# Kernel optimization log

Measured on AMD Instinct MI355X. Metric: run time of the kernel, lower is better.

## Reference

```python
import jax, jax.numpy as jnp
import numpy as np

N_ENT = 50000     # n_entities
C = 128           # channel
N_EDGES = 1600000 # n_edges (avg degree 32)
N_REL = 11        # n_relations; edge_type in [1, N_REL-1]
N_HOPS = 3
EPS = 1e-12       # F.normalize default eps


def setup_inputs() -> dict:
    key = jax.random.key(0)
    k1, k2, k3, k4 = jax.random.split(key, 4)
    entity_emb = jax.random.normal(k1, (N_ENT, C), dtype=jnp.float32)
    edge_index = jax.random.randint(k2, (2, N_EDGES), 0, N_ENT, dtype=jnp.int64)
    edge_type = jax.random.randint(k3, (N_EDGES,), 1, N_REL, dtype=jnp.int64)
    # xavier_uniform bound for (N_REL-1, C)
    bound = float(np.sqrt(6.0 / ((N_REL - 1) + C)))
    weight = jax.random.uniform(k4, (N_REL - 1, C), jnp.float32, -bound, bound)
    return {"entity_emb": entity_emb, "edge_index": edge_index,
            "edge_type": edge_type, "weight": weight}


def reference(entity_emb, edge_index, edge_type, weight):
    head, tail = edge_index[0], edge_index[1]
    # relation embedding per edge: weight[edge_type - 1] -> [E, C]
    rel_emb = weight[edge_type - 1]
    ones = jnp.ones((edge_index.shape[1],), entity_emb.dtype)
    # per-head in-degree counts (constant across hops)
    cnt = jax.ops.segment_sum(ones, head, num_segments=N_ENT)
    denom = jnp.maximum(cnt, 1.0)[:, None]  # scatter_mean: zero rows stay zero

    def hop(emb):
        msg = emb[tail] * rel_emb                                   # gather + mul [E, C]
        agg = jax.ops.segment_sum(msg, head, num_segments=N_ENT) / denom  # scatter_mean
        # F.normalize (L2 per row)
        norm = jnp.linalg.norm(agg, axis=1, keepdims=True)
        return agg / jnp.maximum(norm, EPS)

    res = entity_emb
    emb = entity_emb
    for _ in range(N_HOPS):
        emb = hop(emb)
        res = res + emb
    return res
```

## Files before the change

kernel.cpp:

```cpp
#include <hip/hip_runtime.h>

#define N_ENT   50000
#define CH      128
#define N_EDGES 1600000
#define N_RELM1 10
#define NB      391
#define BCAP    4608
#define BCAP_P  8192
#define PART_BLOCKS 800
#define CHUNK   (N_EDGES / PART_BLOCKS)
#define NRG     (N_ENT / 4)
#define NKEY    512
#define EPS_N   1e-12f

#define RFL(x) __builtin_amdgcn_readfirstlane(x)

__device__ __forceinline__ unsigned int f2bf_bits(float f) {
    unsigned int x = __float_as_uint(f);
    return (x + 0x7FFFu + ((x >> 16) & 1u)) >> 16;
}

__global__ __launch_bounds__(256) void gc_part_kernel(const int* __restrict__ head,
                                                      const int* __restrict__ tail,
                                                      const int* __restrict__ etyp,
                                                      int* __restrict__ barr,
                                                      int* __restrict__ pack,
                                                      const float* __restrict__ ent,
                                                      unsigned int* __restrict__ emb) {
    __shared__ int hist[512];
    __shared__ int boff_s[512];
    __shared__ int fctr[512];
    __shared__ int psum[256];
    __shared__ int stageE[CHUNK];
    __shared__ unsigned short stageB[CHUNK];
    __shared__ int stage2[CHUNK];
    int tid = threadIdx.x, blk = blockIdx.x;
    for (int i = tid; i < 512; i += 256) { hist[i] = 0; fctr[i] = 0; }
    __syncthreads();
    int lo = blk * CHUNK;
    for (int i = tid; i < CHUNK; i += 256) {
        int e = lo + i;
        int h = head[e];
        int b = h >> 7;
        stageE[i] = (tail[e] & 0xFFFF) | ((etyp[e] - 1) << 16) | ((h & 127) << 20);
        stageB[i] = (unsigned short)b;
        atomicAdd(&hist[b], 1);
    }
    __syncthreads();
    int a0 = hist[2 * tid], a1 = hist[2 * tid + 1];
    int s2 = a0 + a1;
    psum[tid] = s2;
    __syncthreads();
    for (int d = 1; d < 256; d <<= 1) {
        int t = (tid >= d) ? psum[tid - d] : 0;
        __syncthreads();
        psum[tid] += t;
        __syncthreads();
    }
    int excl = psum[tid] - s2;
    boff_s[2 * tid] = excl;
    boff_s[2 * tid + 1] = excl + a0;
    __syncthreads();
    for (int i = tid; i < CHUNK; i += 256) {
        int b = stageB[i];
        int pos = boff_s[b] + atomicAdd(&fctr[b], 1);
        stage2[pos] = stageE[i];
    }
    __syncthreads();
    for (int i = tid; i < CHUNK; i += 256) barr[lo + i] = stage2[i];
    for (int i = tid; i < NB; i += 256)
        pack[blk * NB + i] = (boff_s[i] << 8) | fctr[i];
    for (int i = blk * 256 + tid; i < N_ENT * (CH / 2); i += PART_BLOCKS * 256) {
        float2 v = *(const float2*)(ent + 2 * (size_t)i);
        emb[i] = f2bf_bits(v.x) | (f2bf_bits(v.y) << 16);
    }
}

__global__ __launch_bounds__(1024) void gc_place_kernel(const int* __restrict__ barr,
                                                        const int* __restrict__ pack,
                                                        int* __restrict__ deg_arr,
                                                        int* __restrict__ rg_off,
                                                        int* __restrict__ cpk,
                                                        int* __restrict__ csr) {
    __shared__ int ent_s[BCAP];
    __shared__ int psum[1024];
    __shared__ int kcnt[NKEY];
    __shared__ int kctr[NKEY];
    __shared__ int kbase[NKEY];
    int b = blockIdx.x, tid = threadIdx.x;
    if (tid < NKEY) { kcnt[tid] = 0; kctr[tid] = 0; }
    int c = 0, o = 0;
    if (tid < PART_BLOCKS) {
        int pk = pack[tid * NB + b];
        c = pk & 255;
        o = pk >> 8;
    }
    psum[tid] = c;
    __syncthreads();
    for (int d = 1; d < 1024; d <<= 1) {
        int t = (tid >= d) ? psum[tid - d] : 0;
        __syncthreads();
        psum[tid] += t;
        __syncthreads();
    }
    int my_off = psum[tid] - c;
    int n = psum[1023];
    const int* src = barr + tid * CHUNK + o;
    for (int k = 0; k < c; ++k) ent_s[my_off + k] = src[k];
    __syncthreads();
    for (int i = tid; i < n; i += 1024) {
        int e = ent_s[i];
        int hl = (e >> 20) & 127;
        int key = ((hl >> 2) << 4) | (((e >> 14) & 3) << 2) | (hl & 3);
        atomicAdd(&kcnt[key], 1);
    }
    __syncthreads();
    if (tid < 128) {
        int rgl = tid >> 2, r = tid & 3;
        int base = (rgl << 4) | r;
        int c0 = kcnt[base], c1 = kcnt[base + 4], c2 = kcnt[base + 8], c3 = kcnt[base + 12];
        int h = (b << 7) + tid;
        if (h < N_ENT) {
            deg_arr[h] = c0 + c1 + c2 + c3;
            cpk[(((b << 5) + rgl) << 2) + r] =
                ((c0 + 7) >> 3) | (((c1 + 7) >> 3) << 8) |
                (((c2 + 7) >> 3) << 16) | (((c3 + 7) >> 3) << 24);
        }
    }
    int a0 = 0, a1 = 0, s2 = 0;
    if (tid < 256) {
        a0 = (kcnt[2 * tid] + 7) & ~7;
        a1 = (kcnt[2 * tid + 1] + 7) & ~7;
        s2 = a0 + a1;
        psum[tid] = s2;
    }
    __syncthreads();
    for (int d = 1; d < 256; d <<= 1) {
        int t = (tid < 256 && tid >= d) ? psum[tid - d] : 0;
        __syncthreads();
        if (tid < 256) psum[tid] += t;
        __syncthreads();
    }
    if (tid < 256) {
        int excl = psum[tid] - s2;
        kbase[2 * tid] = excl;
        kbase[2 * tid + 1] = excl + a0;
    }
    __syncthreads();
    int lo = b * BCAP_P;
    if (tid < 32) {
        int grg = (b << 5) + tid;
        if (grg < NRG) rg_off[grg] = lo + kbase[tid << 4];
    }
    for (int i = tid; i < n; i += 1024) {
        int e = ent_s[i];
        int hl = (e >> 20) & 127;
        int key = ((hl >> 2) << 4) | (((e >> 14) & 3) << 2) | (hl & 3);
        int pos = lo + kbase[key] + atomicAdd(&kctr[key], 1);
        csr[pos] = e & 0xFFFFF;
    }
    __syncthreads();
    if (tid < NKEY) {
        int cc = kcnt[tid];
        int pc = (cc + 7) & ~7;
        int p0 = lo + kbase[tid];
        for (int k = cc; k < pc; ++k) csr[p0 + k] = 15 << 16;
    }
}

__global__ __launch_bounds__(256, 8) void gc_hop_kernel(
        const unsigned int* __restrict__ src,
        const int* __restrict__ deg_arr,
        const int* __restrict__ rg_off,
        const int* __restrict__ cpk,
        const int* __restrict__ csr,
        const float* __restrict__ wt,
        unsigned int* __restrict__ dst,
        float* __restrict__ res,
        const float* __restrict__ ent,
        const unsigned int* __restrict__ yprev,
        int mode) {
    __shared__ float wt_s[16 * CH];
    for (int i = threadIdx.x; i < 16 * CH; i += 256)
        wt_s[i] = (i < N_RELM1 * CH) ? wt[i] : 0.f;
    __syncthreads();

    int wave = threadIdx.x >> 6, lane = threadIdx.x & 63;
    int rg = RFL(blockIdx.x * 4 + wave);
    if (rg >= NRG) return;

    int4 dd = ((const int4*)deg_arr)[rg];
    int4 cc = ((const int4*)cpk)[rg];
    int segv = rg_off[rg];

    int D0 = RFL(dd.x), D1 = RFL(dd.y), D2 = RFL(dd.z), D3 = RFL(dd.w);
    int C0 = RFL(cc.x), C1 = RFL(cc.y), C2 = RFL(cc.z), C3 = RFL(cc.w);
    int seg = RFL(segv);

    const int4* mp = (const int4*)(csr + seg);
    int4 mB0 = mp[0], mB1 = mp[1];
    mp += 2;

    float ax0 = 0.f, ay0 = 0.f, ax1 = 0.f, ay1 = 0.f;
    float ax2 = 0.f, ay2 = 0.f, ax3 = 0.f, ay3 = 0.f;

    const unsigned* srcl = src + lane;
    const float2*   wl   = (const float2*)wt_s + lane;

#define CHUNK8(axr, ayr) { \
    int p0_ = RFL(mB0.x), p1_ = RFL(mB0.y), p2_ = RFL(mB0.z), p3_ = RFL(mB0.w); \
    int p4_ = RFL(mB1.x), p5_ = RFL(mB1.y), p6_ = RFL(mB1.z), p7_ = RFL(mB1.w); \
    mB0 = mp[0]; mB1 = mp[1]; mp += 2; \
    unsigned v0_ = srcl[(unsigned)(p0_ & 0xFFFF) * 64u]; \
    unsigned v1_ = srcl[(unsigned)(p1_ & 0xFFFF) * 64u]; \
    unsigned v2_ = srcl[(unsigned)(p2_ & 0xFFFF) * 64u]; \
    unsigned v3_ = srcl[(unsigned)(p3_ & 0xFFFF) * 64u]; \
    unsigned v4_ = srcl[(unsigned)(p4_ & 0xFFFF) * 64u]; \
    unsigned v5_ = srcl[(unsigned)(p5_ & 0xFFFF) * 64u]; \
    unsigned v6_ = srcl[(unsigned)(p6_ & 0xFFFF) * 64u]; \
    unsigned v7_ = srcl[(unsigned)(p7_ & 0xFFFF) * 64u]; \
    float2 w0_ = wl[((p0_ >> 16) & 15) * 64]; \
    float2 w1_ = wl[((p1_ >> 16) & 15) * 64]; \
    float2 w2_ = wl[((p2_ >> 16) & 15) * 64]; \
    float2 w3_ = wl[((p3_ >> 16) & 15) * 64]; \
    float2 w4_ = wl[((p4_ >> 16) & 15) * 64]; \
    float2 w5_ = wl[((p5_ >> 16) & 15) * 64]; \
    float2 w6_ = wl[((p6_ >> 16) & 15) * 64]; \
    float2 w7_ = wl[((p7_ >> 16) & 15) * 64]; \
    axr = fmaf(__uint_as_float(v0_ << 16), w0_.x, axr); \
    ayr = fmaf(__uint_as_float(v0_ & 0xFFFF0000u), w0_.y, ayr); \
    axr = fmaf(__uint_as_float(v1_ << 16), w1_.x, axr); \
    ayr = fmaf(__uint_as_float(v1_ & 0xFFFF0000u), w1_.y, ayr); \
    axr = fmaf(__uint_as_float(v2_ << 16), w2_.x, axr); \
    ayr = fmaf(__uint_as_float(v2_ & 0xFFFF0000u), w2_.y, ayr); \
    axr = fmaf(__uint_as_float(v3_ << 16), w3_.x, axr); \
    ayr = fmaf(__uint_as_float(v3_ & 0xFFFF0000u), w3_.y, ayr); \
    axr = fmaf(__uint_as_float(v4_ << 16), w4_.x, axr); \
    ayr = fmaf(__uint_as_float(v4_ & 0xFFFF0000u), w4_.y, ayr); \
    axr = fmaf(__uint_as_float(v5_ << 16), w5_.x, axr); \
    ayr = fmaf(__uint_as_float(v5_ & 0xFFFF0000u), w5_.y, ayr); \
    axr = fmaf(__uint_as_float(v6_ << 16), w6_.x, axr); \
    ayr = fmaf(__uint_as_float(v6_ & 0xFFFF0000u), w6_.y, ayr); \
    axr = fmaf(__uint_as_float(v7_ << 16), w7_.x, axr); \
    ayr = fmaf(__uint_as_float(v7_ & 0xFFFF0000u), w7_.y, ayr); \
}

#define RUN(axr, ayr, Cr) { \
    int n_ = (Cr >> sh) & 255; \
    for (int c_ = 0; c_ < n_; ++c_) CHUNK8(axr, ayr) \
}

    for (int g2 = 0; g2 < 4; ++g2) {
        int sh = g2 << 3;
        RUN(ax0, ay0, C0)
        RUN(ax1, ay1, C1)
        RUN(ax2, ay2, C2)
        RUN(ax3, ay3, C3)
    }
#undef RUN
#undef CHUNK8

#define ROWOUT(r, axr, ayr, Dr) { \
        int row = (rg << 2) + r; \
        float invd = 1.0f / fmaxf((float)Dr, 1.0f); \
        float x0 = axr * invd, x1 = ayr * invd; \
        float s = x0 * x0 + x1 * x1; \
        _Pragma("unroll") \
        for (int o = 32; o; o >>= 1) s += __shfl_xor(s, o, 64); \
        float inv = 1.0f / fmaxf(sqrtf(s), EPS_N); \
        float y0 = x0 * inv, y1v = x1 * inv; \
        if (mode == 0) { \
            dst[(row << 6) + lane] = f2bf_bits(y0) | (f2bf_bits(y1v) << 16); \
        } else { \
            unsigned p1 = yprev[(row << 6) + lane]; \
            unsigned p2 = src[(row << 6) + lane]; \
            int base = (row << 7) + 2 * lane; \
            float2 e = *(const float2*)(ent + base); \
            float2 o2; \
            o2.x = e.x + __uint_as_float(p1 << 16) \
                       + __uint_as_float(p2 << 16) + y0; \
            o2.y = e.y + __uint_as_float(p1 & 0xFFFF0000u) \
                       + __uint_as_float(p2 & 0xFFFF0000u) + y1v; \
            *(float2*)(res + base) = o2; \
        } }

    ROWOUT(0, ax0, ay0, D0);
    ROWOUT(1, ax1, ay1, D1);
    ROWOUT(2, ax2, ay2, D2);
    ROWOUT(3, ax3, ay3, D3);
#undef ROWOUT
}

extern "C" void kernel_launch(void* const* d_in, const int* in_sizes, int n_in,
                              void* d_out, int out_size, void* d_ws, size_t ws_size,
                              hipStream_t stream) {
    const float* ent  = (const float*)d_in[0];
    const int*   eidx = (const int*)d_in[1];
    const int*   etyp = (const int*)d_in[2];
    const float* wt   = (const float*)d_in[3];
    float*       res  = (float*)d_out;

    const int* head = eidx;
    const int* tail = eidx + N_EDGES;

    unsigned int* embA = (unsigned int*)d_ws;
    unsigned int* embB = embA + (size_t)N_ENT * 64;
    int* barr = (int*)embB;
    int* pack = (int*)embB + N_EDGES;
    int* csr     = (int*)(embB + (size_t)N_ENT * 64);
    int* deg_arr = csr + (size_t)NB * BCAP_P;
    int* rg_off  = deg_arr + N_ENT;
    int* cpk     = rg_off + 12544;

    gc_part_kernel<<<PART_BLOCKS, 256, 0, stream>>>(head, tail, etyp, barr, pack,
                                                    ent, embA);
    gc_place_kernel<<<NB, 1024, 0, stream>>>(barr, pack, deg_arr, rg_off, cpk, csr);

    const int hop_grid = NRG / 4;
    gc_hop_kernel<<<hop_grid, 256, 0, stream>>>(embA, deg_arr, rg_off, cpk, csr,
                                                wt, embB, res, ent, embB, 0);
    gc_hop_kernel<<<hop_grid, 256, 0, stream>>>(embB, deg_arr, rg_off, cpk, csr,
                                                wt, embA, res, ent, embB, 0);
    gc_hop_kernel<<<hop_grid, 256, 0, stream>>>(embA, deg_arr, rg_off, cpk, csr,
                                                wt, embB, res, ent, embB, 1);
}
```

Before: 269.0 us.

## Split each wave into two half-waves gathering separate edges with 8-byte loads

The hop kernel now has each half-wave (32 lanes) handle alternating edges. Each lane loads 8 bytes (4 bf16 channels) per edge and reads a float4 of weights, and the two halves are combined with a cross-half shuffle before normalization. Edge padding in the partition kernel drops from multiples of 8 to multiples of 2, which cuts wasted dummy-edge gathers and shrinks the per-bucket capacity. The 8-edge unrolled batch that issued many independent loads is replaced by a 2-edge loop with per-edge scalar metadata loads, so less memory-level parallelism may be in flight per wave. Output writes now use only half the lanes with wider stores.

```diff
diff --git a/kernel.cpp b/kernel.cpp
--- a/kernel.cpp
+++ b/kernel.cpp
@@ -6,7 +6,7 @@
 #define N_RELM1 10
 #define NB      391
 #define BCAP    4608
-#define BCAP_P  8192
+#define BCAP_P  5120
 #define PART_BLOCKS 800
 #define CHUNK   (N_EDGES / PART_BLOCKS)
 #define NRG     (N_ENT / 4)
@@ -123,14 +123,14 @@
         if (h < N_ENT) {
             deg_arr[h] = c0 + c1 + c2 + c3;
             cpk[(((b << 5) + rgl) << 2) + r] =
-                ((c0 + 7) >> 3) | (((c1 + 7) >> 3) << 8) |
-                (((c2 + 7) >> 3) << 16) | (((c3 + 7) >> 3) << 24);
+                ((c0 + 1) >> 1) | (((c1 + 1) >> 1) << 8) |
+                (((c2 + 1) >> 1) << 16) | (((c3 + 1) >> 1) << 24);
         }
     }
     int a0 = 0, a1 = 0, s2 = 0;
     if (tid < 256) {
-        a0 = (kcnt[2 * tid] + 7) & ~7;
-        a1 = (kcnt[2 * tid + 1] + 7) & ~7;
+        a0 = (kcnt[2 * tid] + 1) & ~1;
+        a1 = (kcnt[2 * tid + 1] + 1) & ~1;
         s2 = a0 + a1;
         psum[tid] = s2;
     }
@@ -162,9 +162,7 @@
     __syncthreads();
     if (tid < NKEY) {
         int cc = kcnt[tid];
-        int pc = (cc + 7) & ~7;
-        int p0 = lo + kbase[tid];
-        for (int k = cc; k < pc; ++k) csr[p0 + k] = 15 << 16;
+        if (cc & 1) csr[lo + kbase[tid] + cc] = 15 << 16;
     }
 }
 
@@ -197,97 +195,86 @@
     int C0 = RFL(cc.x), C1 = RFL(cc.y), C2 = RFL(cc.z), C3 = RFL(cc.w);
     int seg = RFL(segv);
 
-    const int4* mp = (const int4*)(csr + seg);
-    int4 mB0 = mp[0], mB1 = mp[1];
-    mp += 2;
-
-    float ax0 = 0.f, ay0 = 0.f, ax1 = 0.f, ay1 = 0.f;
-    float ax2 = 0.f, ay2 = 0.f, ax3 = 0.f, ay3 = 0.f;
-
-    const unsigned* srcl = src + lane;
-    const float2*   wl   = (const float2*)wt_s + lane;
-
-#define CHUNK8(axr, ayr) { \
-    int p0_ = RFL(mB0.x), p1_ = RFL(mB0.y), p2_ = RFL(mB0.z), p3_ = RFL(mB0.w); \
-    int p4_ = RFL(mB1.x), p5_ = RFL(mB1.y), p6_ = RFL(mB1.z), p7_ = RFL(mB1.w); \
-    mB0 = mp[0]; mB1 = mp[1]; mp += 2; \
-    unsigned v0_ = srcl[(unsigned)(p0_ & 0xFFFF) * 64u]; \
-    unsigned v1_ = srcl[(unsigned)(p1_ & 0xFFFF) * 64u]; \
-    unsigned v2_ = srcl[(unsigned)(p2_ & 0xFFFF) * 64u]; \
-    unsigned v3_ = srcl[(unsigned)(p3_ & 0xFFFF) * 64u]; \
-    unsigned v4_ = srcl[(unsigned)(p4_ & 0xFFFF) * 64u]; \
-    unsigned v5_ = srcl[(unsigned)(p5_ & 0xFFFF) * 64u]; \
-    unsigned v6_ = srcl[(unsigned)(p6_ & 0xFFFF) * 64u]; \
-    unsigned v7_ = srcl[(unsigned)(p7_ & 0xFFFF) * 64u]; \
-    float2 w0_ = wl[((p0_ >> 16) & 15) * 64]; \
-    float2 w1_ = wl[((p1_ >> 16) & 15) * 64]; \
-    float2 w2_ = wl[((p2_ >> 16) & 15) * 64]; \
-    float2 w3_ = wl[((p3_ >> 16) & 15) * 64]; \
-    float2 w4_ = wl[((p4_ >> 16) & 15) * 64]; \
-    float2 w5_ = wl[((p5_ >> 16) & 15) * 64]; \
-    float2 w6_ = wl[((p6_ >> 16) & 15) * 64]; \
-    float2 w7_ = wl[((p7_ >> 16) & 15) * 64]; \
-    axr = fmaf(__uint_as_float(v0_ << 16), w0_.x, axr); \
-    ayr = fmaf(__uint_as_float(v0_ & 0xFFFF0000u), w0_.y, ayr); \
-    axr = fmaf(__uint_as_float(v1_ << 16), w1_.x, axr); \
-    ayr = fmaf(__uint_as_float(v1_ & 0xFFFF0000u), w1_.y, ayr); \
-    axr = fmaf(__uint_as_float(v2_ << 16), w2_.x, axr); \
-    ayr = fmaf(__uint_as_float(v2_ & 0xFFFF0000u), w2_.y, ayr); \
-    axr = fmaf(__uint_as_float(v3_ << 16), w3_.x, axr); \
-    ayr = fmaf(__uint_as_float(v3_ & 0xFFFF0000u), w3_.y, ayr); \
-    axr = fmaf(__uint_as_float(v4_ << 16), w4_.x, axr); \
-    ayr = fmaf(__uint_as_float(v4_ & 0xFFFF0000u), w4_.y, ayr); \
-    axr = fmaf(__uint_as_float(v5_ << 16), w5_.x, axr); \
-    ayr = fmaf(__uint_as_float(v5_ & 0xFFFF0000u), w5_.y, ayr); \
-    axr = fmaf(__uint_as_float(v6_ << 16), w6_.x, axr); \
-    ayr = fmaf(__uint_as_float(v6_ & 0xFFFF0000u), w6_.y, ayr); \
-    axr = fmaf(__uint_as_float(v7_ << 16), w7_.x, axr); \
-    ayr = fmaf(__uint_as_float(v7_ & 0xFFFF0000u), w7_.y, ayr); \
-}
-
-#define RUN(axr, ayr, Cr) { \
-    int n_ = (Cr >> sh) & 255; \
-    for (int c_ = 0; c_ < n_; ++c_) CHUNK8(axr, ayr) \
-}
+    int l31 = lane & 31;
+    int half = lane >> 5;
+    const char* srcb = (const char*)src;
+    int goff = l31 * 8;
+    const float* wrow = wt_s + l31 * 4;
+    int mofs = (seg + half) * 4;
+    const char* csrb = (const char*)csr;
+
+    float a00 = 0.f, a01 = 0.f, a02 = 0.f, a03 = 0.f;
+    float a10 = 0.f, a11 = 0.f, a12 = 0.f, a13 = 0.f;
+    float a20 = 0.f, a21 = 0.f, a22 = 0.f, a23 = 0.f;
+    float a30 = 0.f, a31 = 0.f, a32 = 0.f, a33 = 0.f;
+
+#define PAIR(A0, A1, A2, A3) { \
+    int m_ = *(const int*)(csrb + mofs); mofs += 8; \
+    uint2 v_ = *(const uint2*)(srcb + (unsigned)(m_ & 0xFFFF) * 256u + goff); \
+    float4 w_ = *(const float4*)(wrow + ((m_ >> 16) & 15) * CH); \
+    A0 = fmaf(__uint_as_float(v_.x << 16), w_.x, A0); \
+    A1 = fmaf(__uint_as_float(v_.x & 0xFFFF0000u), w_.y, A1); \
+    A2 = fmaf(__uint_as_float(v_.y << 16), w_.z, A2); \
+    A3 = fmaf(__uint_as_float(v_.y & 0xFFFF0000u), w_.w, A3); }
+
+#define RUN(A0, A1, A2, A3, Cr) { \
+    int np_ = (Cr >> sh) & 255; \
+    int k_ = 0; \
+    for (; k_ + 2 <= np_; k_ += 2) { PAIR(A0, A1, A2, A3) PAIR(A0, A1, A2, A3) } \
+    if (k_ < np_) { PAIR(A0, A1, A2, A3) } }
 
     for (int g2 = 0; g2 < 4; ++g2) {
         int sh = g2 << 3;
-        RUN(ax0, ay0, C0)
-        RUN(ax1, ay1, C1)
-        RUN(ax2, ay2, C2)
-        RUN(ax3, ay3, C3)
+        RUN(a00, a01, a02, a03, C0)
+        RUN(a10, a11, a12, a13, C1)
+        RUN(a20, a21, a22, a23, C2)
+        RUN(a30, a31, a32, a33, C3)
     }
 #undef RUN
-#undef CHUNK8
-
-#define ROWOUT(r, axr, ayr, Dr) { \
+#undef PAIR
+
+#define ROWOUT(r, A0, A1, A2, A3, Dr) { \
         int row = (rg << 2) + r; \
+        A0 += __shfl_xor(A0, 32, 64); \
+        A1 += __shfl_xor(A1, 32, 64); \
+        A2 += __shfl_xor(A2, 32, 64); \
+        A3 += __shfl_xor(A3, 32, 64); \
         float invd = 1.0f / fmaxf((float)Dr, 1.0f); \
-        float x0 = axr * invd, x1 = ayr * invd; \
-        float s = x0 * x0 + x1 * x1; \
+        float x0 = A0 * invd, x1 = A1 * invd, x2 = A2 * invd, x3 = A3 * invd; \
+        float s = x0 * x0 + x1 * x1 + x2 * x2 + x3 * x3; \
         _Pragma("unroll") \
         for (int o = 32; o; o >>= 1) s += __shfl_xor(s, o, 64); \
+        s *= 0.5f;    \
         float inv = 1.0f / fmaxf(sqrtf(s), EPS_N); \
-        float y0 = x0 * inv, y1v = x1 * inv; \
-        if (mode == 0) { \
-            dst[(row << 6) + lane] = f2bf_bits(y0) | (f2bf_bits(y1v) << 16); \
-        } else { \
-            unsigned p1 = yprev[(row << 6) + lane]; \
-            unsigned p2 = src[(row << 6) + lane]; \
-            int base = (row << 7) + 2 * lane; \
-            float2 e = *(const float2*)(ent + base); \
-            float2 o2; \
-            o2.x = e.x + __uint_as_float(p1 << 16) \
-                       + __uint_as_float(p2 << 16) + y0; \
-            o2.y = e.y + __uint_as_float(p1 & 0xFFFF0000u) \
-                       + __uint_as_float(p2 & 0xFFFF0000u) + y1v; \
-            *(float2*)(res + base) = o2; \
+        float y0 = x0 * inv, y1 = x1 * inv, y2 = x2 * inv, y3 = x3 * inv; \
+        if (lane < 32) { \
+            int idx = (row << 5) + l31; \
+            if (mode == 0) { \
+                uint2 u; \
+                u.x = f2bf_bits(y0) | (f2bf_bits(y1) << 16); \
+                u.y = f2bf_bits(y2) | (f2bf_bits(y3) << 16); \
+                ((uint2*)dst)[idx] = u; \
+            } else { \
+                uint2 p1 = ((const uint2*)yprev)[idx]; \
+                uint2 p2 = ((const uint2*)src)[idx]; \
+                float4 e = ((const float4*)ent)[idx]; \
+                float4 o2; \
+                o2.x = e.x + __uint_as_float(p1.x << 16) \
+                           + __uint_as_float(p2.x << 16) + y0; \
+                o2.y = e.y + __uint_as_float(p1.x & 0xFFFF0000u) \
+                           + __uint_as_float(p2.x & 0xFFFF0000u) + y1; \
+                o2.z = e.z + __uint_as_float(p1.y << 16) \
+                           + __uint_as_float(p2.y << 16) + y2; \
+                o2.w = e.w + __uint_as_float(p1.y & 0xFFFF0000u) \
+                           + __uint_as_float(p2.y & 0xFFFF0000u) + y3; \
+                ((float4*)res)[idx] = o2; \
+            } \
         } }
 
-    ROWOUT(0, ax0, ay0, D0);
-    ROWOUT(1, ax1, ay1, D1);
-    ROWOUT(2, ax2, ay2, D2);
-    ROWOUT(3, ax3, ay3, D3);
+    ROWOUT(0, a00, a01, a02, a03, D0);
+    ROWOUT(1, a10, a11, a12, a13, D1);
+    ROWOUT(2, a20, a21, a22, a23, D2);
+    ROWOUT(3, a30, a31, a32, a33, D3);
 #undef ROWOUT
 }
 
```

Result: slower. 283.7 us (+5.5%).

## Pad CSR segments to 4 edges and use wave-shuffle scans in place kernel

Applied to the files above, without the earlier changes.

Reduces per-key edge padding from multiples of 8 to multiples of 4, so the hop kernel processes 4-edge chunks and does less padded dummy gather work (about 2 fewer dummy edges per segment on average). The block capacity per bucket shrinks to match. The shared-memory Hillis-Steele scans in the place kernel are replaced with wave-level shuffle scans plus a small cross-wave sum, cutting barriers. In exchange, each chunk now issues fewer independent gathers, and the loop no longer prefetches the next index vector, which may reduce memory-level parallelism.

```diff
diff --git a/kernel.cpp b/kernel.cpp
--- a/kernel.cpp
+++ b/kernel.cpp
@@ -6,7 +6,7 @@
 #define N_RELM1 10
 #define NB      391
 #define BCAP    4608
-#define BCAP_P  8192
+#define BCAP_P  6144
 #define PART_BLOCKS 800
 #define CHUNK   (N_EDGES / PART_BLOCKS)
 #define NRG     (N_ENT / 4)
@@ -83,11 +83,13 @@
                                                         int* __restrict__ cpk,
                                                         int* __restrict__ csr) {
     __shared__ int ent_s[BCAP];
-    __shared__ int psum[1024];
     __shared__ int kcnt[NKEY];
     __shared__ int kctr[NKEY];
     __shared__ int kbase[NKEY];
+    __shared__ int wsum[16];
+    __shared__ int wsum2[4];
     int b = blockIdx.x, tid = threadIdx.x;
+    int lane = tid & 63, wv = tid >> 6;
     if (tid < NKEY) { kcnt[tid] = 0; kctr[tid] = 0; }
     int c = 0, o = 0;
     if (tid < PART_BLOCKS) {
@@ -95,16 +97,22 @@
         c = pk & 255;
         o = pk >> 8;
     }
-    psum[tid] = c;
-    __syncthreads();
-    for (int d = 1; d < 1024; d <<= 1) {
-        int t = (tid >= d) ? psum[tid - d] : 0;
-        __syncthreads();
-        psum[tid] += t;
-        __syncthreads();
-    }
-    int my_off = psum[tid] - c;
-    int n = psum[1023];
+    int inc = c;
+    #pragma unroll
+    for (int d = 1; d < 64; d <<= 1) {
+        int t = __shfl_up(inc, d, 64);
+        if (lane >= d) inc += t;
+    }
+    if (lane == 63) wsum[wv] = inc;
+    __syncthreads();
+    int woff = 0, n = 0;
+    #pragma unroll
+    for (int i = 0; i < 16; ++i) {
+        int w = wsum[i];
+        woff += (i < wv) ? w : 0;
+        n += w;
+    }
+    int my_off = woff + inc - c;
     const int* src = barr + tid * CHUNK + o;
     for (int k = 0; k < c; ++k) ent_s[my_off + k] = src[k];
     __syncthreads();
@@ -118,31 +126,35 @@
     if (tid < 128) {
         int rgl = tid >> 2, r = tid & 3;
         int base = (rgl << 4) | r;
-        int c0 = kcnt[base], c1 = kcnt[base + 4], c2 = kcnt[base + 8], c3 = kcnt[base + 12];
+        int c0 = kcnt[base], c1 = kcnt[base + 4];
+        int c2 = kcnt[base + 8], c3 = kcnt[base + 12];
         int h = (b << 7) + tid;
         if (h < N_ENT) {
             deg_arr[h] = c0 + c1 + c2 + c3;
             cpk[(((b << 5) + rgl) << 2) + r] =
-                ((c0 + 7) >> 3) | (((c1 + 7) >> 3) << 8) |
-                (((c2 + 7) >> 3) << 16) | (((c3 + 7) >> 3) << 24);
+                ((c0 + 3) >> 2) | (((c1 + 3) >> 2) << 8) |
+                (((c2 + 3) >> 2) << 16) | (((c3 + 3) >> 2) << 24);
         }
     }
-    int a0 = 0, a1 = 0, s2 = 0;
+    int a0 = 0, s2 = 0, inc2 = 0;
     if (tid < 256) {
-        a0 = (kcnt[2 * tid] + 7) & ~7;
-        a1 = (kcnt[2 * tid + 1] + 7) & ~7;
+        a0 = (kcnt[2 * tid] + 3) & ~3;
+        int a1 = (kcnt[2 * tid + 1] + 3) & ~3;
         s2 = a0 + a1;
-        psum[tid] = s2;
-    }
-    __syncthreads();
-    for (int d = 1; d < 256; d <<= 1) {
-        int t = (tid < 256 && tid >= d) ? psum[tid - d] : 0;
-        __syncthreads();
-        if (tid < 256) psum[tid] += t;
-        __syncthreads();
-    }
+        inc2 = s2;
+        #pragma unroll
+        for (int d = 1; d < 64; d <<= 1) {
+            int t = __shfl_up(inc2, d, 64);
+            if (lane >= d) inc2 += t;
+        }
+        if (lane == 63) wsum2[wv] = inc2;
+    }
+    __syncthreads();
     if (tid < 256) {
-        int excl = psum[tid] - s2;
+        int woff2 = 0;
+        #pragma unroll
+        for (int i = 0; i < 4; ++i) woff2 += (i < wv) ? wsum2[i] : 0;
+        int excl = woff2 + inc2 - s2;
         kbase[2 * tid] = excl;
         kbase[2 * tid + 1] = excl + a0;
     }
@@ -162,7 +174,7 @@
     __syncthreads();
     if (tid < NKEY) {
         int cc = kcnt[tid];
-        int pc = (cc + 7) & ~7;
+        int pc = (cc + 3) & ~3;
         int p0 = lo + kbase[tid];
         for (int k = cc; k < pc; ++k) csr[p0 + k] = 15 << 16;
     }
@@ -198,8 +210,6 @@
     int seg = RFL(segv);
 
     const int4* mp = (const int4*)(csr + seg);
-    int4 mB0 = mp[0], mB1 = mp[1];
-    mp += 2;
 
     float ax0 = 0.f, ay0 = 0.f, ax1 = 0.f, ay1 = 0.f;
     float ax2 = 0.f, ay2 = 0.f, ax3 = 0.f, ay3 = 0.f;
@@ -207,26 +217,17 @@
     const unsigned* srcl = src + lane;
     const float2*   wl   = (const float2*)wt_s + lane;
 
-#define CHUNK8(axr, ayr) { \
-    int p0_ = RFL(mB0.x), p1_ = RFL(mB0.y), p2_ = RFL(mB0.z), p3_ = RFL(mB0.w); \
-    int p4_ = RFL(mB1.x), p5_ = RFL(mB1.y), p6_ = RFL(mB1.z), p7_ = RFL(mB1.w); \
-    mB0 = mp[0]; mB1 = mp[1]; mp += 2; \
+#define CHUNK4(axr, ayr) { \
+    int4 m_ = mp[0]; mp += 1; \
+    int p0_ = RFL(m_.x), p1_ = RFL(m_.y), p2_ = RFL(m_.z), p3_ = RFL(m_.w); \
     unsigned v0_ = srcl[(unsigned)(p0_ & 0xFFFF) * 64u]; \
     unsigned v1_ = srcl[(unsigned)(p1_ & 0xFFFF) * 64u]; \
     unsigned v2_ = srcl[(unsigned)(p2_ & 0xFFFF) * 64u]; \
     unsigned v3_ = srcl[(unsigned)(p3_ & 0xFFFF) * 64u]; \
-    unsigned v4_ = srcl[(unsigned)(p4_ & 0xFFFF) * 64u]; \
-    unsigned v5_ = srcl[(unsigned)(p5_ & 0xFFFF) * 64u]; \
-    unsigned v6_ = srcl[(unsigned)(p6_ & 0xFFFF) * 64u]; \
-    unsigned v7_ = srcl[(unsigned)(p7_ & 0xFFFF) * 64u]; \
     float2 w0_ = wl[((p0_ >> 16) & 15) * 64]; \
     float2 w1_ = wl[((p1_ >> 16) & 15) * 64]; \
     float2 w2_ = wl[((p2_ >> 16) & 15) * 64]; \
     float2 w3_ = wl[((p3_ >> 16) & 15) * 64]; \
-    float2 w4_ = wl[((p4_ >> 16) & 15) * 64]; \
-    float2 w5_ = wl[((p5_ >> 16) & 15) * 64]; \
-    float2 w6_ = wl[((p6_ >> 16) & 15) * 64]; \
-    float2 w7_ = wl[((p7_ >> 16) & 15) * 64]; \
     axr = fmaf(__uint_as_float(v0_ << 16), w0_.x, axr); \
     ayr = fmaf(__uint_as_float(v0_ & 0xFFFF0000u), w0_.y, ayr); \
     axr = fmaf(__uint_as_float(v1_ << 16), w1_.x, axr); \
@@ -235,19 +236,11 @@
     ayr = fmaf(__uint_as_float(v2_ & 0xFFFF0000u), w2_.y, ayr); \
     axr = fmaf(__uint_as_float(v3_ << 16), w3_.x, axr); \
     ayr = fmaf(__uint_as_float(v3_ & 0xFFFF0000u), w3_.y, ayr); \
-    axr = fmaf(__uint_as_float(v4_ << 16), w4_.x, axr); \
-    ayr = fmaf(__uint_as_float(v4_ & 0xFFFF0000u), w4_.y, ayr); \
-    axr = fmaf(__uint_as_float(v5_ << 16), w5_.x, axr); \
-    ayr = fmaf(__uint_as_float(v5_ & 0xFFFF0000u), w5_.y, ayr); \
-    axr = fmaf(__uint_as_float(v6_ << 16), w6_.x, axr); \
-    ayr = fmaf(__uint_as_float(v6_ & 0xFFFF0000u), w6_.y, ayr); \
-    axr = fmaf(__uint_as_float(v7_ << 16), w7_.x, axr); \
-    ayr = fmaf(__uint_as_float(v7_ & 0xFFFF0000u), w7_.y, ayr); \
 }
 
 #define RUN(axr, ayr, Cr) { \
     int n_ = (Cr >> sh) & 255; \
-    for (int c_ = 0; c_ < n_; ++c_) CHUNK8(axr, ayr) \
+    for (int c_ = 0; c_ < n_; ++c_) CHUNK4(axr, ayr) \
 }
 
     for (int g2 = 0; g2 < 4; ++g2) {
@@ -258,7 +251,7 @@
         RUN(ax3, ay3, C3)
     }
 #undef RUN
-#undef CHUNK8
+#undef CHUNK4
 
 #define ROWOUT(r, axr, ayr, Dr) { \
         int row = (rg << 2) + r; \
```

Result: no change. 271.5 us (+0.9%).
